# Performance work log

Hardware: AMD Instinct MI355X
Metric: run time of the kernel (lower is better)

The kernel has to match this reference:

```python
import jax, jax.numpy as jnp
import numpy as np

NUM_USERS = 1024          # == user_feature_dim, per the module's num_users = user_proj.in_features
NUM_BUSINESS = 100000
N = NUM_USERS + NUM_BUSINESS
E = 2000000
FEAT = 1024
H = [128, 128, 128, 64]


def setup_inputs() -> dict:
    key = jax.random.key(0)
    ks = jax.random.split(key, 13)
    s = lambda fan_in: 1.0 / np.sqrt(fan_in)
    return {
        "x": jax.random.normal(ks[0], (N, FEAT), dtype=jnp.float32),
        "edge_index": jax.random.randint(ks[1], (2, E), 0, N, dtype=jnp.int32),
        "Wu": jax.random.normal(ks[2], (FEAT, H[0]), dtype=jnp.float32) * s(FEAT),
        "bu": jax.random.normal(ks[3], (H[0],), dtype=jnp.float32) * s(FEAT),
        "Wb": jax.random.normal(ks[4], (FEAT, H[0]), dtype=jnp.float32) * s(FEAT),
        "bb": jax.random.normal(ks[5], (H[0],), dtype=jnp.float32) * s(FEAT),
        "W1": jax.random.normal(ks[6], (H[0], H[1]), dtype=jnp.float32) * s(H[0]),
        "b1": jax.random.normal(ks[7], (H[1],), dtype=jnp.float32) * s(H[0]),
        "W2": jax.random.normal(ks[8], (H[1], H[2]), dtype=jnp.float32) * s(H[1]),
        "b2": jax.random.normal(ks[9], (H[2],), dtype=jnp.float32) * s(H[1]),
        "W3": jax.random.normal(ks[10], (H[2], H[3]), dtype=jnp.float32) * s(H[2]),
        "b3": jax.random.normal(ks[11], (H[3],), dtype=jnp.float32) * s(H[2]),
    }


def gcn_conv(h, W, b, src, dst, norm, num_nodes):
    # PyG GCNConv: out = D^-1/2 (A+I) D^-1/2 (h W) + b
    hw = h @ W                                   # [N, out]
    msg = hw[src] * norm[:, None]                # [E+N, out]
    out = jax.ops.segment_sum(msg, dst, num_segments=num_nodes)
    return out + b


def gcn_norm(edge_index, num_nodes, dtype):
    loop = jnp.arange(num_nodes, dtype=edge_index.dtype)
    src = jnp.concatenate([edge_index[0], loop])  # add self loops
    dst = jnp.concatenate([edge_index[1], loop])
    deg = jax.ops.segment_sum(jnp.ones(src.shape, dtype=dtype), dst, num_segments=num_nodes)
    dinv = jnp.where(deg > 0, jax.lax.rsqrt(deg), 0.0)
    norm = dinv[src] * dinv[dst]
    return src, dst, norm


def reference(x, edge_index, Wu, bu, Wb, bb, W1, b1, W2, b2, W3, b3):
    # split by num_users = user_proj.in_features (as in the source)
    user_h = x[:NUM_USERS] @ Wu + bu
    business_h = x[NUM_USERS:] @ Wb + bb
    h = jnp.concatenate([user_h, business_h], axis=0)  # [N, H0]

    src, dst, norm = gcn_norm(edge_index, N, h.dtype)

    h = jax.nn.relu(gcn_conv(h, W1, b1, src, dst, norm, N))  # dropout = identity (eval)
    h = jax.nn.relu(gcn_conv(h, W2, b2, src, dst, norm, N))
    h = gcn_conv(h, W3, b3, src, dst, norm, N)
    return h
```

## Files before the change

kernel.cpp:

```cpp
#include <hip/hip_runtime.h>
#include <stdint.h>

typedef __attribute__((ext_vector_type(8))) short bf16x8;
typedef __attribute__((ext_vector_type(4))) float f32x4;

constexpr int FEATC = 1024;
constexpr int H0 = 128;

static inline int ceil_div(int a, int b){ return (a + b - 1) / b; }

__device__ inline ushort f2bf_rne(float f) {
    uint u = __float_as_uint(f);
    uint r = (u + 0x7FFFu + ((u >> 16) & 1u)) >> 16;
    return (ushort)r;
}
__device__ inline float bf2f(ushort h) { return __uint_as_float(((uint)h) << 16); }
__device__ inline uint pack2(ushort a, ushort b) { return (uint)a | ((uint)b << 16); }


__global__ __launch_bounds__(256) void init_kernel(int* __restrict__ cnt, int* __restrict__ fill, int n) {
    int i = blockIdx.x * 256 + threadIdx.x;
    if (i < n) { cnt[i] = 0; fill[i] = 0; }
}

__global__ __launch_bounds__(256) void count_kernel(const int* __restrict__ ei, int* __restrict__ cnt, int E) {
    int e = blockIdx.x * 256 + threadIdx.x;
    if (e < E) atomicAdd(&cnt[ei[E + e]], 1);
}

__global__ __launch_bounds__(256) void dinv_kernel(const int* __restrict__ cnt, float* __restrict__ dinv, int n) {
    int i = blockIdx.x * 256 + threadIdx.x;
    if (i < n) dinv[i] = rsqrtf((float)(cnt[i] + 1));
}

__global__ __launch_bounds__(1024) void scan_kernel(const int* __restrict__ cnt, int* __restrict__ rowptr, int n) {
    __shared__ int wsum[16];
    __shared__ int carry_s;
    const int tid = threadIdx.x;
    const int lane = tid & 63, wid = tid >> 6;
    if (tid == 0) carry_s = 0;
    __syncthreads();
    for (int base = 0; base < n; base += 1024) {
        int idx = base + tid;
        int v = (idx < n) ? cnt[idx] : 0;
        int s = v;
        #pragma unroll
        for (int off = 1; off < 64; off <<= 1) {
            int t = __shfl_up(s, off, 64);
            if (lane >= off) s += t;
        }
        if (lane == 63) wsum[wid] = s;
        __syncthreads();
        if (wid == 0) {
            int ws = (lane < 16) ? wsum[lane] : 0;
            #pragma unroll
            for (int off = 1; off < 16; off <<= 1) {
                int t = __shfl_up(ws, off, 64);
                if (lane >= off) ws += t;
            }
            if (lane < 16) wsum[lane] = ws;
        }
        __syncthreads();
        int carry = carry_s;
        if (idx < n) rowptr[idx] = carry + (wid ? wsum[wid - 1] : 0) + s - v;
        __syncthreads();
        if (tid == 1023) carry_s = carry + wsum[15];
        __syncthreads();
    }
    if (tid == 0) rowptr[n] = carry_s;
}

__global__ __launch_bounds__(256) void fill_kernel(const int* __restrict__ ei, const int* __restrict__ rowptr,
                                                   int* __restrict__ fill, int* __restrict__ adj, int E) {
    int e = blockIdx.x * 256 + threadIdx.x;
    if (e < E) {
        int d = ei[E + e];
        int pos = rowptr[d] + atomicAdd(&fill[d], 1);
        adj[pos] = ei[e];
    }
}

__global__ __launch_bounds__(256) void pack_w_kernel(const float* __restrict__ W, ushort* __restrict__ hi,
                                                     ushort* __restrict__ lo, int K, int N) {
    int o = blockIdx.x * 256 + threadIdx.x;
    if (o >= K * N) return;
    int nn = o / K, kk = o - nn * K;
    float f = W[(size_t)kk * N + nn];
    ushort h = f2bf_rne(f);
    float fl = f - bf2f(h);
    hi[o] = h;
    lo[o] = f2bf_rne(fl);
}

template<int NCOLS, bool BIAS, bool SPLIT>
__global__ __launch_bounds__(NCOLS == 128 ? 512 : 256) void mfma_gemm_kernel(
    const float* __restrict__ A, int lda, int K, int n,
    const ushort* __restrict__ WtHiA, const ushort* __restrict__ WtLoA,
    const ushort* __restrict__ WtHiB, const ushort* __restrict__ WtLoB,
    const float* __restrict__ biasA, const float* __restrict__ biasB,
    float* __restrict__ C)
{
    constexpr int BM = 128, BK = 64;
    constexpr int WN = NCOLS / 64;
    constexpr int THREADS = 4 * WN * 64;
    constexpr int ASTEPS = (BM * BK / 4) / THREADS;
    constexpr int BSTEPS = (NCOLS * BK / 8) / THREADS;

    __shared__ alignas(16) ushort Ahi[BM * BK], Alo[BM * BK];
    __shared__ alignas(16) ushort Bhi[NCOLS * BK], Blo[NCOLS * BK];

    const int tid = threadIdx.x;
    const int row0 = blockIdx.x * BM;
    const ushort* WtHi = (SPLIT && row0 >= 1024) ? WtHiB : WtHiA;
    const ushort* WtLo = (SPLIT && row0 >= 1024) ? WtLoB : WtLoA;
    const float*  bias = (SPLIT && row0 >= 1024) ? biasB : biasA;

    const int wave = tid >> 6, lane = tid & 63;
    const int wn = wave % WN, wm = wave / WN;
    const int r15 = lane & 15, g = lane >> 4;

    f32x4 acc[2][4];
    #pragma unroll
    for (int i = 0; i < 2; ++i)
        #pragma unroll
        for (int j = 0; j < 4; ++j) acc[i][j] = (f32x4){0.f, 0.f, 0.f, 0.f};

    for (int k0 = 0; k0 < K; k0 += BK) {
        __syncthreads();
        #pragma unroll
        for (int ii = 0; ii < ASTEPS; ++ii) {
            int chunk = tid + ii * THREADS;
            int r = chunk >> 4, c = chunk & 15;
            int grow = row0 + r;
            float4 v = make_float4(0.f, 0.f, 0.f, 0.f);
            if (grow < n) v = *reinterpret_cast<const float4*>(A + (size_t)grow * lda + k0 + c * 4);
            ushort h0 = f2bf_rne(v.x), h1 = f2bf_rne(v.y), h2 = f2bf_rne(v.z), h3 = f2bf_rne(v.w);
            ushort l0 = f2bf_rne(v.x - bf2f(h0)), l1 = f2bf_rne(v.y - bf2f(h1));
            ushort l2 = f2bf_rne(v.z - bf2f(h2)), l3 = f2bf_rne(v.w - bf2f(h3));
            int bo = r * 128 + c * 8;
            int sw = bo ^ (((bo >> 7) & 7) << 4);
            *reinterpret_cast<uint2*>((char*)Ahi + sw) = make_uint2(pack2(h0, h1), pack2(h2, h3));
            *reinterpret_cast<uint2*>((char*)Alo + sw) = make_uint2(pack2(l0, l1), pack2(l2, l3));
        }
        #pragma unroll
        for (int ii = 0; ii < BSTEPS; ++ii) {
            int chunk = tid + ii * THREADS;
            int r = chunk >> 3, gg = chunk & 7;
            bf16x8 hv = *reinterpret_cast<const bf16x8*>(WtHi + (size_t)r * K + k0 + gg * 8);
            bf16x8 lv = *reinterpret_cast<const bf16x8*>(WtLo + (size_t)r * K + k0 + gg * 8);
            int bo = r * 128 + gg * 16;
            int sw = bo ^ (((bo >> 7) & 7) << 4);
            *reinterpret_cast<bf16x8*>((char*)Bhi + sw) = hv;
            *reinterpret_cast<bf16x8*>((char*)Blo + sw) = lv;
        }
        __syncthreads();
        #pragma unroll
        for (int ks = 0; ks < 2; ++ks) {
            bf16x8 ah[2], al[2], bh[4], bl[4];
            #pragma unroll
            for (int mi = 0; mi < 2; ++mi) {
                int row = wm * 32 + mi * 16 + r15;
                int bo = row * 128 + ks * 64 + g * 16;
                int sw = bo ^ (((bo >> 7) & 7) << 4);
                ah[mi] = *reinterpret_cast<const bf16x8*>((const char*)Ahi + sw);
                al[mi] = *reinterpret_cast<const bf16x8*>((const char*)Alo + sw);
            }
            #pragma unroll
            for (int ni = 0; ni < 4; ++ni) {
                int row = wn * 64 + ni * 16 + r15;
                int bo = row * 128 + ks * 64 + g * 16;
                int sw = bo ^ (((bo >> 7) & 7) << 4);
                bh[ni] = *reinterpret_cast<const bf16x8*>((const char*)Bhi + sw);
                bl[ni] = *reinterpret_cast<const bf16x8*>((const char*)Blo + sw);
            }
            #pragma unroll
            for (int mi = 0; mi < 2; ++mi)
                #pragma unroll
                for (int ni = 0; ni < 4; ++ni) {
                    acc[mi][ni] = __builtin_amdgcn_mfma_f32_16x16x32_bf16(ah[mi], bh[ni], acc[mi][ni], 0, 0, 0);
                    acc[mi][ni] = __builtin_amdgcn_mfma_f32_16x16x32_bf16(ah[mi], bl[ni], acc[mi][ni], 0, 0, 0);
                    acc[mi][ni] = __builtin_amdgcn_mfma_f32_16x16x32_bf16(al[mi], bh[ni], acc[mi][ni], 0, 0, 0);
                }
        }
    }
    #pragma unroll
    for (int mi = 0; mi < 2; ++mi)
        #pragma unroll
        for (int ni = 0; ni < 4; ++ni) {
            int col = wn * 64 + ni * 16 + r15;
            float bv = BIAS ? bias[col] : 0.f;
            #pragma unroll
            for (int r = 0; r < 4; ++r) {
                int grow = row0 + wm * 32 + mi * 16 + g * 4 + r;
                if (grow < n) C[(size_t)grow * NCOLS + col] = acc[mi][ni][r] + bv;
            }
        }
}

template<int COLS, bool RELU>
__global__ __launch_bounds__(256) void agg_kernel(
    const float* __restrict__ hw, const float* __restrict__ dinv,
    const int* __restrict__ rowptr, const int* __restrict__ adj,
    const float* __restrict__ bias, float* __restrict__ out, int n)
{
    const int node = (int)((blockIdx.x * (size_t)blockDim.x + threadIdx.x) >> 6);
    const int lane = threadIdx.x & 63;
    if (node >= n) return;
    const int beg = rowptr[node], end = rowptr[node + 1];
    const float di = dinv[node];

    if (COLS == 128) {
        float acc0 = 0.f, acc1 = 0.f;
        int e = beg;
        for (; e + 1 < end; e += 2) {
            int s0 = adj[e], s1 = adj[e + 1];
            float w0 = dinv[s0], w1 = dinv[s1];
            float2 r0 = *reinterpret_cast<const float2*>(hw + (size_t)s0 * 128 + 2 * lane);
            float2 r1 = *reinterpret_cast<const float2*>(hw + (size_t)s1 * 128 + 2 * lane);
            acc0 += w0 * r0.x; acc1 += w0 * r0.y;
            acc0 += w1 * r1.x; acc1 += w1 * r1.y;
        }
        if (e < end) {
            int s0 = adj[e];
            float w0 = dinv[s0];
            float2 r0 = *reinterpret_cast<const float2*>(hw + (size_t)s0 * 128 + 2 * lane);
            acc0 += w0 * r0.x; acc1 += w0 * r0.y;
        }
        float2 self = *reinterpret_cast<const float2*>(hw + (size_t)node * 128 + 2 * lane);
        float v0 = di * acc0 + di * di * self.x + bias[2 * lane + 0];
        float v1 = di * acc1 + di * di * self.y + bias[2 * lane + 1];
        if (RELU) { v0 = fmaxf(v0, 0.f); v1 = fmaxf(v1, 0.f); }
        *reinterpret_cast<float2*>(out + (size_t)node * 128 + 2 * lane) = make_float2(v0, v1);
    } else {
        float acc0 = 0.f;
        int e = beg;
        for (; e + 1 < end; e += 2) {
            int s0 = adj[e], s1 = adj[e + 1];
            float w0 = dinv[s0], w1 = dinv[s1];
            float r0 = hw[(size_t)s0 * COLS + lane];
            float r1 = hw[(size_t)s1 * COLS + lane];
            acc0 += w0 * r0 + w1 * r1;
        }
        if (e < end) {
            int s0 = adj[e];
            acc0 += dinv[s0] * hw[(size_t)s0 * COLS + lane];
        }
        float self = hw[(size_t)node * COLS + lane];
        float v0 = di * acc0 + di * di * self + bias[lane];
        if (RELU) v0 = fmaxf(v0, 0.f);
        out[(size_t)node * COLS + lane] = v0;
    }
}


extern "C" void kernel_launch(void* const* d_in, const int* in_sizes, int n_in,
                              void* d_out, int out_size, void* d_ws, size_t ws_size,
                              hipStream_t stream) {
    const float* x  = (const float*)d_in[0];
    const int*   ei = (const int*)  d_in[1];
    const float* Wu = (const float*)d_in[2];
    const float* bu = (const float*)d_in[3];
    const float* Wb = (const float*)d_in[4];
    const float* bb = (const float*)d_in[5];
    const float* W1 = (const float*)d_in[6];
    const float* b1 = (const float*)d_in[7];
    const float* W2 = (const float*)d_in[8];
    const float* b2 = (const float*)d_in[9];
    const float* W3 = (const float*)d_in[10];
    const float* b3 = (const float*)d_in[11];
    float* out = (float*)d_out;

    const int N_ = in_sizes[0] / FEATC;
    const int E_ = in_sizes[1] / 2;

    size_t off = 0;
    auto carve = [&](size_t bytes) -> void* {
        void* p = (char*)d_ws + off;
        off += (bytes + 255) & ~(size_t)255;
        return p;
    };
    float*  buf0   = (float*) carve((size_t)N_ * H0 * sizeof(float));
    float*  buf1   = (float*) carve((size_t)N_ * H0 * sizeof(float));
    float*  dinv   = (float*) carve((size_t)N_ * sizeof(float));
    int*    cnt    = (int*)   carve((size_t)N_ * sizeof(int));
    int*    fillc  = (int*)   carve((size_t)N_ * sizeof(int));
    int*    rowptr = (int*)   carve(((size_t)N_ + 1) * sizeof(int));
    int*    adj    = (int*)   carve((size_t)E_ * sizeof(int));
    ushort* wtu_hi = (ushort*)carve((size_t)1024 * 128 * 2);
    ushort* wtu_lo = (ushort*)carve((size_t)1024 * 128 * 2);
    ushort* wtb_hi = (ushort*)carve((size_t)1024 * 128 * 2);
    ushort* wtb_lo = (ushort*)carve((size_t)1024 * 128 * 2);
    ushort* wt1_hi = (ushort*)carve((size_t)128 * 128 * 2);
    ushort* wt1_lo = (ushort*)carve((size_t)128 * 128 * 2);
    ushort* wt2_hi = (ushort*)carve((size_t)128 * 128 * 2);
    ushort* wt2_lo = (ushort*)carve((size_t)128 * 128 * 2);
    ushort* wt3_hi = (ushort*)carve((size_t)128 * 64 * 2);
    ushort* wt3_lo = (ushort*)carve((size_t)128 * 64 * 2);

    pack_w_kernel<<<ceil_div(1024 * 128, 256), 256, 0, stream>>>(Wu, wtu_hi, wtu_lo, 1024, 128);
    pack_w_kernel<<<ceil_div(1024 * 128, 256), 256, 0, stream>>>(Wb, wtb_hi, wtb_lo, 1024, 128);
    pack_w_kernel<<<ceil_div(128 * 128, 256), 256, 0, stream>>>(W1, wt1_hi, wt1_lo, 128, 128);
    pack_w_kernel<<<ceil_div(128 * 128, 256), 256, 0, stream>>>(W2, wt2_hi, wt2_lo, 128, 128);
    pack_w_kernel<<<ceil_div(128 * 64, 256), 256, 0, stream>>>(W3, wt3_hi, wt3_lo, 128, 64);

    init_kernel<<<ceil_div(N_, 256), 256, 0, stream>>>(cnt, fillc, N_);
    count_kernel<<<ceil_div(E_, 256), 256, 0, stream>>>(ei, cnt, E_);
    dinv_kernel<<<ceil_div(N_, 256), 256, 0, stream>>>(cnt, dinv, N_);
    scan_kernel<<<1, 1024, 0, stream>>>(cnt, rowptr, N_);
    fill_kernel<<<ceil_div(E_, 256), 256, 0, stream>>>(ei, rowptr, fillc, adj, E_);

    const int gemm_grid = ceil_div(N_, 128);
    const int agg_grid  = ceil_div(N_, 4);

    mfma_gemm_kernel<128, true, true><<<gemm_grid, 512, 0, stream>>>(
        x, 1024, 1024, N_, wtu_hi, wtu_lo, wtb_hi, wtb_lo, bu, bb, buf0);
    mfma_gemm_kernel<128, false, false><<<gemm_grid, 512, 0, stream>>>(
        buf0, 128, 128, N_, wt1_hi, wt1_lo, wt1_hi, wt1_lo, nullptr, nullptr, buf1);
    agg_kernel<128, true><<<agg_grid, 256, 0, stream>>>(buf1, dinv, rowptr, adj, b1, buf0, N_);
    mfma_gemm_kernel<128, false, false><<<gemm_grid, 512, 0, stream>>>(
        buf0, 128, 128, N_, wt2_hi, wt2_lo, wt2_hi, wt2_lo, nullptr, nullptr, buf1);
    agg_kernel<128, true><<<agg_grid, 256, 0, stream>>>(buf1, dinv, rowptr, adj, b2, buf0, N_);
    mfma_gemm_kernel<64, false, false><<<gemm_grid, 256, 0, stream>>>(
        buf0, 128, 128, N_, wt3_hi, wt3_lo, wt3_hi, wt3_lo, nullptr, nullptr, buf1);
    agg_kernel<64, false><<<agg_grid, 256, 0, stream>>>(buf1, dinv, rowptr, adj, b3, out, N_);
}
```

Before: 1.467 ms.

## Pre-scale GEMM output by dinv, store activations as bf16 hi/lo, parallelize scan

The GEMMs now fold the source-side dinv scaling into their epilogue, so the aggregation kernels no longer gather dinv per neighbor and treat the self loop as one more term. Intermediate activations are written as split bf16 hi/lo pairs by the producers, which lets the next GEMM load them directly instead of converting fp32 to hi/lo in its A-tile load. The single-block serial scan is replaced by a three-kernel block-parallel scan, and the aggregation loop is unrolled by 4. The bf16 conversion now goes through the HIP intrinsic. These changes add launches and extra hi/lo output stores in exchange for removing per-edge dinv gathers and repeated A-tile conversion.

```diff
diff --git a/kernel.cpp b/kernel.cpp
--- a/kernel.cpp
+++ b/kernel.cpp
@@ -1,4 +1,5 @@
 #include <hip/hip_runtime.h>
+#include <hip/hip_bf16.h>
 #include <stdint.h>
 
 typedef __attribute__((ext_vector_type(8))) short bf16x8;
@@ -9,12 +10,13 @@
 
 static inline int ceil_div(int a, int b){ return (a + b - 1) / b; }
 
-__device__ inline ushort f2bf_rne(float f) {
-    uint u = __float_as_uint(f);
-    uint r = (u + 0x7FFFu + ((u >> 16) & 1u)) >> 16;
-    return (ushort)r;
-}
-__device__ inline float bf2f(ushort h) { return __uint_as_float(((uint)h) << 16); }
+__device__ inline ushort f2bf(float f) {
+    __hip_bfloat16 h = __float2bfloat16(f);
+    union { __hip_bfloat16 h; ushort u; } c;
+    c.h = h;
+    return c.u;
+}
+__device__ inline float bf2f(ushort u) { return __uint_as_float(((uint)u) << 16); }
 __device__ inline uint pack2(ushort a, ushort b) { return (uint)a | ((uint)b << 16); }
 
 
@@ -33,41 +35,60 @@
     if (i < n) dinv[i] = rsqrtf((float)(cnt[i] + 1));
 }
 
-__global__ __launch_bounds__(1024) void scan_kernel(const int* __restrict__ cnt, int* __restrict__ rowptr, int n) {
-    __shared__ int wsum[16];
-    __shared__ int carry_s;
-    const int tid = threadIdx.x;
-    const int lane = tid & 63, wid = tid >> 6;
-    if (tid == 0) carry_s = 0;
+__global__ __launch_bounds__(256) void scan_a_kernel(const int* __restrict__ cnt, int* __restrict__ rowptr,
+                                                     int* __restrict__ bsum, int n) {
+    __shared__ int wsum_[4];
+    const int tid = threadIdx.x, lane = tid & 63, wid = tid >> 6;
+    const int base = blockIdx.x * 1024 + tid * 4;
+    int4 v = make_int4(0, 0, 0, 0);
+    if (base + 3 < n) v = *reinterpret_cast<const int4*>(cnt + base);
+    else {
+        if (base     < n) v.x = cnt[base];
+        if (base + 1 < n) v.y = cnt[base + 1];
+        if (base + 2 < n) v.z = cnt[base + 2];
+        if (base + 3 < n) v.w = cnt[base + 3];
+    }
+    const int tsum = v.x + v.y + v.z + v.w;
+    int s = tsum;
+    #pragma unroll
+    for (int off = 1; off < 64; off <<= 1) { int t = __shfl_up(s, off, 64); if (lane >= off) s += t; }
+    if (lane == 63) wsum_[wid] = s;
     __syncthreads();
-    for (int base = 0; base < n; base += 1024) {
-        int idx = base + tid;
-        int v = (idx < n) ? cnt[idx] : 0;
-        int s = v;
+    const int woff = (wid > 0 ? wsum_[0] : 0) + (wid > 1 ? wsum_[1] : 0) + (wid > 2 ? wsum_[2] : 0);
+    const int excl = woff + s - tsum;
+    if (base     < n) rowptr[base]     = excl;
+    if (base + 1 < n) rowptr[base + 1] = excl + v.x;
+    if (base + 2 < n) rowptr[base + 2] = excl + v.x + v.y;
+    if (base + 3 < n) rowptr[base + 3] = excl + v.x + v.y + v.z;
+    if (tid == 255) bsum[blockIdx.x] = woff + s;
+}
+
+__global__ __launch_bounds__(256) void scan_b_kernel(int* __restrict__ bsum, int* __restrict__ rowptr, int n, int B) {
+    __shared__ int wsum_[4];
+    const int tid = threadIdx.x, lane = tid & 63, wid = tid >> 6;
+    const int v = (tid < B) ? bsum[tid] : 0;
+    int s = v;
+    #pragma unroll
+    for (int off = 1; off < 64; off <<= 1) { int t = __shfl_up(s, off, 64); if (lane >= off) s += t; }
+    if (lane == 63) wsum_[wid] = s;
+    __syncthreads();
+    const int woff = (wid > 0 ? wsum_[0] : 0) + (wid > 1 ? wsum_[1] : 0) + (wid > 2 ? wsum_[2] : 0);
+    const int excl = woff + s - v;
+    if (tid < B) bsum[tid] = excl;
+    if (tid == 255) rowptr[n] = woff + s;
+}
+
+__global__ __launch_bounds__(256) void scan_c_kernel(int* __restrict__ rowptr, const int* __restrict__ bsum, int n) {
+    const int add = bsum[blockIdx.x];
+    const int base = blockIdx.x * 1024 + threadIdx.x * 4;
+    if (base + 3 < n) {
+        int4 t = *reinterpret_cast<int4*>(rowptr + base);
+        t.x += add; t.y += add; t.z += add; t.w += add;
+        *reinterpret_cast<int4*>(rowptr + base) = t;
+    } else {
         #pragma unroll
-        for (int off = 1; off < 64; off <<= 1) {
-            int t = __shfl_up(s, off, 64);
-            if (lane >= off) s += t;
-        }
-        if (lane == 63) wsum[wid] = s;
-        __syncthreads();
-        if (wid == 0) {
-            int ws = (lane < 16) ? wsum[lane] : 0;
-            #pragma unroll
-            for (int off = 1; off < 16; off <<= 1) {
-                int t = __shfl_up(ws, off, 64);
-                if (lane >= off) ws += t;
-            }
-            if (lane < 16) wsum[lane] = ws;
-        }
-        __syncthreads();
-        int carry = carry_s;
-        if (idx < n) rowptr[idx] = carry + (wid ? wsum[wid - 1] : 0) + s - v;
-        __syncthreads();
-        if (tid == 1023) carry_s = carry + wsum[15];
-        __syncthreads();
-    }
-    if (tid == 0) rowptr[n] = carry_s;
+        for (int k = 0; k < 4; ++k) if (base + k < n) rowptr[base + k] += add;
+    }
 }
 
 __global__ __launch_bounds__(256) void fill_kernel(const int* __restrict__ ei, const int* __restrict__ rowptr,
@@ -86,26 +107,24 @@
     if (o >= K * N) return;
     int nn = o / K, kk = o - nn * K;
     float f = W[(size_t)kk * N + nn];
-    ushort h = f2bf_rne(f);
-    float fl = f - bf2f(h);
+    ushort h = f2bf(f);
     hi[o] = h;
-    lo[o] = f2bf_rne(fl);
-}
-
-template<int NCOLS, bool BIAS, bool SPLIT>
+    lo[o] = f2bf(f - bf2f(h));
+}
+
+template<int NCOLS, bool SPLIT, bool A_F32, bool BIAS, bool OUT_BF16, bool DINV>
 __global__ __launch_bounds__(NCOLS == 128 ? 512 : 256) void mfma_gemm_kernel(
-    const float* __restrict__ A, int lda, int K, int n,
+    const float* __restrict__ Af, const ushort* __restrict__ AhiG, const ushort* __restrict__ AloG,
+    int lda, int K, int n,
     const ushort* __restrict__ WtHiA, const ushort* __restrict__ WtLoA,
     const ushort* __restrict__ WtHiB, const ushort* __restrict__ WtLoB,
     const float* __restrict__ biasA, const float* __restrict__ biasB,
-    float* __restrict__ C)
+    const float* __restrict__ dinv,
+    float* __restrict__ Cf, ushort* __restrict__ Chi, ushort* __restrict__ Clo)
 {
     constexpr int BM = 128, BK = 64;
     constexpr int WN = NCOLS / 64;
     constexpr int THREADS = 4 * WN * 64;
-    constexpr int ASTEPS = (BM * BK / 4) / THREADS;
-    constexpr int BSTEPS = (NCOLS * BK / 8) / THREADS;
-
     __shared__ alignas(16) ushort Ahi[BM * BK], Alo[BM * BK];
     __shared__ alignas(16) ushort Bhi[NCOLS * BK], Blo[NCOLS * BK];
 
@@ -127,31 +146,56 @@
 
     for (int k0 = 0; k0 < K; k0 += BK) {
         __syncthreads();
-        #pragma unroll
-        for (int ii = 0; ii < ASTEPS; ++ii) {
-            int chunk = tid + ii * THREADS;
-            int r = chunk >> 4, c = chunk & 15;
-            int grow = row0 + r;
-            float4 v = make_float4(0.f, 0.f, 0.f, 0.f);
-            if (grow < n) v = *reinterpret_cast<const float4*>(A + (size_t)grow * lda + k0 + c * 4);
-            ushort h0 = f2bf_rne(v.x), h1 = f2bf_rne(v.y), h2 = f2bf_rne(v.z), h3 = f2bf_rne(v.w);
-            ushort l0 = f2bf_rne(v.x - bf2f(h0)), l1 = f2bf_rne(v.y - bf2f(h1));
-            ushort l2 = f2bf_rne(v.z - bf2f(h2)), l3 = f2bf_rne(v.w - bf2f(h3));
-            int bo = r * 128 + c * 8;
-            int sw = bo ^ (((bo >> 7) & 7) << 4);
-            *reinterpret_cast<uint2*>((char*)Ahi + sw) = make_uint2(pack2(h0, h1), pack2(h2, h3));
-            *reinterpret_cast<uint2*>((char*)Alo + sw) = make_uint2(pack2(l0, l1), pack2(l2, l3));
-        }
-        #pragma unroll
-        for (int ii = 0; ii < BSTEPS; ++ii) {
-            int chunk = tid + ii * THREADS;
-            int r = chunk >> 3, gg = chunk & 7;
-            bf16x8 hv = *reinterpret_cast<const bf16x8*>(WtHi + (size_t)r * K + k0 + gg * 8);
-            bf16x8 lv = *reinterpret_cast<const bf16x8*>(WtLo + (size_t)r * K + k0 + gg * 8);
-            int bo = r * 128 + gg * 16;
-            int sw = bo ^ (((bo >> 7) & 7) << 4);
-            *reinterpret_cast<bf16x8*>((char*)Bhi + sw) = hv;
-            *reinterpret_cast<bf16x8*>((char*)Blo + sw) = lv;
+        if constexpr (A_F32) {
+            constexpr int ASTEPS = (BM * BK / 4) / THREADS;
+            #pragma unroll
+            for (int ii = 0; ii < ASTEPS; ++ii) {
+                int chunk = tid + ii * THREADS;
+                int r = chunk >> 4, c = chunk & 15;
+                int grow = row0 + r;
+                float4 v = make_float4(0.f, 0.f, 0.f, 0.f);
+                if (grow < n) v = *reinterpret_cast<const float4*>(Af + (size_t)grow * lda + k0 + c * 4);
+                ushort h0 = f2bf(v.x), h1 = f2bf(v.y), h2 = f2bf(v.z), h3 = f2bf(v.w);
+                float l0 = v.x - bf2f(h0), l1 = v.y - bf2f(h1);
+                float l2 = v.z - bf2f(h2), l3 = v.w - bf2f(h3);
+                uint2 hu = make_uint2(pack2(h0, h1), pack2(h2, h3));
+                uint2 lu = make_uint2(pack2(f2bf(l0), f2bf(l1)), pack2(f2bf(l2), f2bf(l3)));
+                int bo = r * 128 + c * 8;
+                int sw = bo ^ (((bo >> 7) & 7) << 4);
+                *reinterpret_cast<uint2*>((char*)Ahi + sw) = hu;
+                *reinterpret_cast<uint2*>((char*)Alo + sw) = lu;
+            }
+        } else {
+            constexpr int ASTEPS = (BM * BK / 8) / THREADS;
+            #pragma unroll
+            for (int ii = 0; ii < ASTEPS; ++ii) {
+                int chunk = tid + ii * THREADS;
+                int r = chunk >> 3, c = chunk & 7;
+                int grow = row0 + r;
+                bf16x8 hv{}, lv{};
+                if (grow < n) {
+                    hv = *reinterpret_cast<const bf16x8*>(AhiG + (size_t)grow * lda + k0 + c * 8);
+                    lv = *reinterpret_cast<const bf16x8*>(AloG + (size_t)grow * lda + k0 + c * 8);
+                }
+                int bo = r * 128 + c * 16;
+                int sw = bo ^ (((bo >> 7) & 7) << 4);
+                *reinterpret_cast<bf16x8*>((char*)Ahi + sw) = hv;
+                *reinterpret_cast<bf16x8*>((char*)Alo + sw) = lv;
+            }
+        }
+        {
+            constexpr int BSTEPS = (NCOLS * BK / 8) / THREADS;
+            #pragma unroll
+            for (int ii = 0; ii < BSTEPS; ++ii) {
+                int chunk = tid + ii * THREADS;
+                int r = chunk >> 3, c = chunk & 7;
+                bf16x8 hv = *reinterpret_cast<const bf16x8*>(WtHi + (size_t)r * K + k0 + c * 8);
+                bf16x8 lv = *reinterpret_cast<const bf16x8*>(WtLo + (size_t)r * K + k0 + c * 8);
+                int bo = r * 128 + c * 16;
+                int sw = bo ^ (((bo >> 7) & 7) << 4);
+                *reinterpret_cast<bf16x8*>((char*)Bhi + sw) = hv;
+                *reinterpret_cast<bf16x8*>((char*)Blo + sw) = lv;
+            }
         }
         __syncthreads();
         #pragma unroll
@@ -192,16 +236,27 @@
             #pragma unroll
             for (int r = 0; r < 4; ++r) {
                 int grow = row0 + wm * 32 + mi * 16 + g * 4 + r;
-                if (grow < n) C[(size_t)grow * NCOLS + col] = acc[mi][ni][r] + bv;
-            }
-        }
-}
-
-template<int COLS, bool RELU>
+                if (grow < n) {
+                    float v = acc[mi][ni][r] + bv;
+                    if (DINV) v *= dinv[grow];
+                    if (OUT_BF16) {
+                        ushort h = f2bf(v);
+                        Chi[(size_t)grow * NCOLS + col] = h;
+                        Clo[(size_t)grow * NCOLS + col] = f2bf(v - bf2f(h));
+                    } else {
+                        Cf[(size_t)grow * NCOLS + col] = v;
+                    }
+                }
+            }
+        }
+}
+
+template<int COLS, bool RELU, bool OUT_BF16>
 __global__ __launch_bounds__(256) void agg_kernel(
     const float* __restrict__ hw, const float* __restrict__ dinv,
     const int* __restrict__ rowptr, const int* __restrict__ adj,
-    const float* __restrict__ bias, float* __restrict__ out, int n)
+    const float* __restrict__ bias, float* __restrict__ outF,
+    ushort* __restrict__ outHi, ushort* __restrict__ outLo, int n)
 {
     const int node = (int)((blockIdx.x * (size_t)blockDim.x + threadIdx.x) >> 6);
     const int lane = threadIdx.x & 63;
@@ -210,45 +265,50 @@
     const float di = dinv[node];
 
     if (COLS == 128) {
-        float acc0 = 0.f, acc1 = 0.f;
+        float2 self = *reinterpret_cast<const float2*>(hw + (size_t)node * 128 + 2 * lane);
+        float acc0 = self.x, acc1 = self.y;
         int e = beg;
-        for (; e + 1 < end; e += 2) {
-            int s0 = adj[e], s1 = adj[e + 1];
-            float w0 = dinv[s0], w1 = dinv[s1];
+        for (; e + 3 < end; e += 4) {
+            int s0 = adj[e], s1 = adj[e + 1], s2 = adj[e + 2], s3 = adj[e + 3];
             float2 r0 = *reinterpret_cast<const float2*>(hw + (size_t)s0 * 128 + 2 * lane);
             float2 r1 = *reinterpret_cast<const float2*>(hw + (size_t)s1 * 128 + 2 * lane);
-            acc0 += w0 * r0.x; acc1 += w0 * r0.y;
-            acc0 += w1 * r1.x; acc1 += w1 * r1.y;
-        }
-        if (e < end) {
+            float2 r2 = *reinterpret_cast<const float2*>(hw + (size_t)s2 * 128 + 2 * lane);
+            float2 r3 = *reinterpret_cast<const float2*>(hw + (size_t)s3 * 128 + 2 * lane);
+            acc0 += r0.x + r1.x + r2.x + r3.x;
+            acc1 += r0.y + r1.y + r2.y + r3.y;
+        }
+        for (; e < end; ++e) {
             int s0 = adj[e];
-            float w0 = dinv[s0];
             float2 r0 = *reinterpret_cast<const float2*>(hw + (size_t)s0 * 128 + 2 * lane);
-            acc0 += w0 * r0.x; acc1 += w0 * r0.y;
-        }
-        float2 self = *reinterpret_cast<const float2*>(hw + (size_t)node * 128 + 2 * lane);
-        float v0 = di * acc0 + di * di * self.x + bias[2 * lane + 0];
-        float v1 = di * acc1 + di * di * self.y + bias[2 * lane + 1];
+            acc0 += r0.x; acc1 += r0.y;
+        }
+        float2 bv = *reinterpret_cast<const float2*>(bias + 2 * lane);
+        float v0 = di * acc0 + bv.x;
+        float v1 = di * acc1 + bv.y;
         if (RELU) { v0 = fmaxf(v0, 0.f); v1 = fmaxf(v1, 0.f); }
-        *reinterpret_cast<float2*>(out + (size_t)node * 128 + 2 * lane) = make_float2(v0, v1);
+        if (OUT_BF16) {
+            ushort h0 = f2bf(v0), h1 = f2bf(v1);
+            *reinterpret_cast<uint*>(outHi + (size_t)node * 128 + 2 * lane) = pack2(h0, h1);
+            *reinterpret_cast<uint*>(outLo + (size_t)node * 128 + 2 * lane) =
+                pack2(f2bf(v0 - bf2f(h0)), f2bf(v1 - bf2f(h1)));
+        } else {
+            *reinterpret_cast<float2*>(outF + (size_t)node * 128 + 2 * lane) = make_float2(v0, v1);
+        }
     } else {
-        float acc0 = 0.f;
+        float acc0 = hw[(size_t)node * COLS + lane];
         int e = beg;
-        for (; e + 1 < end; e += 2) {
-            int s0 = adj[e], s1 = adj[e + 1];
-            float w0 = dinv[s0], w1 = dinv[s1];
+        for (; e + 3 < end; e += 4) {
+            int s0 = adj[e], s1 = adj[e + 1], s2 = adj[e + 2], s3 = adj[e + 3];
             float r0 = hw[(size_t)s0 * COLS + lane];
             float r1 = hw[(size_t)s1 * COLS + lane];
-            acc0 += w0 * r0 + w1 * r1;
-        }
-        if (e < end) {
-            int s0 = adj[e];
-            acc0 += dinv[s0] * hw[(size_t)s0 * COLS + lane];
-        }
-        float self = hw[(size_t)node * COLS + lane];
-        float v0 = di * acc0 + di * di * self + bias[lane];
+            float r2 = hw[(size_t)s2 * COLS + lane];
+            float r3 = hw[(size_t)s3 * COLS + lane];
+            acc0 += r0 + r1 + r2 + r3;
+        }
+        for (; e < end; ++e) acc0 += hw[(size_t)adj[e] * COLS + lane];
+        float v0 = di * acc0 + bias[lane];
         if (RELU) v0 = fmaxf(v0, 0.f);
-        out[(size_t)node * COLS + lane] = v0;
+        outF[(size_t)node * COLS + lane] = v0;
     }
 }
 
@@ -272,6 +332,7 @@
 
     const int N_ = in_sizes[0] / FEATC;
     const int E_ = in_sizes[1] / 2;
+    const int SB = ceil_div(N_, 1024);
 
     size_t off = 0;
     auto carve = [&](size_t bytes) -> void* {
@@ -279,12 +340,14 @@
         off += (bytes + 255) & ~(size_t)255;
         return p;
     };
-    float*  buf0   = (float*) carve((size_t)N_ * H0 * sizeof(float));
-    float*  buf1   = (float*) carve((size_t)N_ * H0 * sizeof(float));
+    float*  bufF   = (float*) carve((size_t)N_ * H0 * sizeof(float));
+    ushort* hHi    = (ushort*)carve((size_t)N_ * H0 * 2);
+    ushort* hLo    = (ushort*)carve((size_t)N_ * H0 * 2);
     float*  dinv   = (float*) carve((size_t)N_ * sizeof(float));
     int*    cnt    = (int*)   carve((size_t)N_ * sizeof(int));
     int*    fillc  = (int*)   carve((size_t)N_ * sizeof(int));
     int*    rowptr = (int*)   carve(((size_t)N_ + 1) * sizeof(int));
+    int*    bsum   = (int*)   carve(256 * sizeof(int));
     int*    adj    = (int*)   carve((size_t)E_ * sizeof(int));
     ushort* wtu_hi = (ushort*)carve((size_t)1024 * 128 * 2);
     ushort* wtu_lo = (ushort*)carve((size_t)1024 * 128 * 2);
@@ -306,21 +369,30 @@
     init_kernel<<<ceil_div(N_, 256), 256, 0, stream>>>(cnt, fillc, N_);
     count_kernel<<<ceil_div(E_, 256), 256, 0, stream>>>(ei, cnt, E_);
     dinv_kernel<<<ceil_div(N_, 256), 256, 0, stream>>>(cnt, dinv, N_);
-    scan_kernel<<<1, 1024, 0, stream>>>(cnt, rowptr, N_);
+    scan_a_kernel<<<SB, 256, 0, stream>>>(cnt, rowptr, bsum, N_);
+    scan_b_kernel<<<1, 256, 0, stream>>>(bsum, rowptr, N_, SB);
+    scan_c_kernel<<<SB, 256, 0, stream>>>(rowptr, bsum, N_);
     fill_kernel<<<ceil_div(E_, 256), 256, 0, stream>>>(ei, rowptr, fillc, adj, E_);
 
     const int gemm_grid = ceil_div(N_, 128);
     const int agg_grid  = ceil_div(N_, 4);
 
-    mfma_gemm_kernel<128, true, true><<<gemm_grid, 512, 0, stream>>>(
-        x, 1024, 1024, N_, wtu_hi, wtu_lo, wtb_hi, wtb_lo, bu, bb, buf0);
-    mfma_gemm_kernel<128, false, false><<<gemm_grid, 512, 0, stream>>>(
-        buf0, 128, 128, N_, wt1_hi, wt1_lo, wt1_hi, wt1_lo, nullptr, nullptr, buf1);
-    agg_kernel<128, true><<<agg_grid, 256, 0, stream>>>(buf1, dinv, rowptr, adj, b1, buf0, N_);
-    mfma_gemm_kernel<128, false, false><<<gemm_grid, 512, 0, stream>>>(
-        buf0, 128, 128, N_, wt2_hi, wt2_lo, wt2_hi, wt2_lo, nullptr, nullptr, buf1);
-    agg_kernel<128, true><<<agg_grid, 256, 0, stream>>>(buf1, dinv, rowptr, adj, b2, buf0, N_);
-    mfma_gemm_kernel<64, false, false><<<gemm_grid, 256, 0, stream>>>(
-        buf0, 128, 128, N_, wt3_hi, wt3_lo, wt3_hi, wt3_lo, nullptr, nullptr, buf1);
-    agg_kernel<64, false><<<agg_grid, 256, 0, stream>>>(buf1, dinv, rowptr, adj, b3, out, N_);
-}
+    mfma_gemm_kernel<128, true, true, true, true, false><<<gemm_grid, 512, 0, stream>>>(
+        x, nullptr, nullptr, 1024, 1024, N_,
+        wtu_hi, wtu_lo, wtb_hi, wtb_lo, bu, bb, nullptr, nullptr, hHi, hLo);
+    mfma_gemm_kernel<128, false, false, false, false, true><<<gemm_grid, 512, 0, stream>>>(
+        nullptr, hHi, hLo, 128, 128, N_,
+        wt1_hi, wt1_lo, wt1_hi, wt1_lo, nullptr, nullptr, dinv, bufF, nullptr, nullptr);
+    agg_kernel<128, true, true><<<agg_grid, 256, 0, stream>>>(
+        bufF, dinv, rowptr, adj, b1, nullptr, hHi, hLo, N_);
+    mfma_gemm_kernel<128, false, false, false, false, true><<<gemm_grid, 512, 0, stream>>>(
+        nullptr, hHi, hLo, 128, 128, N_,
+        wt2_hi, wt2_lo, wt2_hi, wt2_lo, nullptr, nullptr, dinv, bufF, nullptr, nullptr);
+    agg_kernel<128, true, true><<<agg_grid, 256, 0, stream>>>(
+        bufF, dinv, rowptr, adj, b2, nullptr, hHi, hLo, N_);
+    mfma_gemm_kernel<64, false, false, false, false, true><<<gemm_grid, 256, 0, stream>>>(
+        nullptr, hHi, hLo, 128, 128, N_,
+        wt3_hi, wt3_lo, wt3_hi, wt3_lo, nullptr, nullptr, dinv, bufF, nullptr, nullptr);
+    agg_kernel<64, false, false><<<agg_grid, 256, 0, stream>>>(
+        bufF, dinv, rowptr, adj, b3, out, nullptr, nullptr, N_);
+}
```

After: 1.289 ms. -12.1%, faster.
